# Performance work log

Measured on AMD Instinct MI355X. Metric: run time of the kernel, lower is better.

The kernel has to match this reference:

```python
import jax, jax.numpy as jnp
import numpy as np

N, D_IN, D_OUT = 8192, 768, 64

def setup_inputs() -> dict:
    key = jax.random.key(0)
    k1, k2, k3, k4 = jax.random.split(key, 4)
    x = jax.random.normal(k1, (N, D_IN), dtype=jnp.float32)
    # nn.Linear weight is [d_out, d_in]; we store transposed [d_in, d_out] for x @ W
    s = 1.0 / np.sqrt(D_IN)
    Wk = jax.random.normal(k2, (D_IN, D_OUT), dtype=jnp.float32) * s
    Wq = jax.random.normal(k3, (D_IN, D_OUT), dtype=jnp.float32) * s
    Wv = jax.random.normal(k4, (D_IN, D_OUT), dtype=jnp.float32) * s
    return {"x": x, "Wk": Wk, "Wq": Wq, "Wv": Wv}

def reference(x, Wk, Wq, Wv):
    inv_sqrt_dk = 1.0 / np.sqrt(D_OUT)
    # Faithful to source: k_w output used as the left matrix, q_w output as right
    wq = x @ Wk            # [N, d_out]  (source: weighted_q = k_w(x))
    wk = x @ Wq            # [N, d_out]  (source: weighted_k = q_w(x))
    scores = wq @ wk.T     # [N, N]
    attn = jax.nn.softmax(scores * inv_sqrt_dk, axis=-1)
    wv = x @ Wv            # [N, d_out]
    return attn @ wv       # [N, d_out]
```

## Files before the change

kernel.cpp:

```cpp
#include <hip/hip_runtime.h>
#include <hip/hip_bf16.h>

#define NTOK 8192
#define DIN  768

typedef float  f32x4  __attribute__((ext_vector_type(4)));
typedef float  f32x16 __attribute__((ext_vector_type(16)));
typedef short  bf16x8 __attribute__((ext_vector_type(8)));

static __device__ __forceinline__ unsigned short f2bf(float f) {
  unsigned int u = __float_as_uint(f);
  u += 0x7FFFu + ((u >> 16) & 1u);
  return (unsigned short)(u >> 16);
}
static __device__ __forceinline__ unsigned cvt_pk(float lo, float hi) {
  unsigned r;
  asm("v_cvt_pk_bf16_f32 %0, %1, %2" : "=v"(r) : "v"(lo), "v"(hi));
  return r;
}
static __device__ __forceinline__ void pswap(unsigned &x, unsigned &y) {
  auto r = __builtin_amdgcn_permlane32_swap(x, y, false, false);
  x = r[0]; y = r[1];
}

union U4 { unsigned u[4]; bf16x8 v; uint4 q; };

__global__ __launch_bounds__(256) void prep_wf(
    const float* __restrict__ Wk, const float* __restrict__ Wq,
    const float* __restrict__ Wv, unsigned short* __restrict__ Wf) {
  int tid  = blockIdx.x * 256 + threadIdx.x;
  int lane = tid & 63;
  int chunk = tid >> 6;
  int g = chunk / 24, kt = chunk - g * 24;
  int col = (g & 3) * 16 + (lane & 15);
  int k0  = kt * 32 + ((lane >> 4) & 3) * 8;
  int ws  = g >> 2;
  const float* W = (ws == 0) ? Wk : (ws == 1) ? Wq : Wv;
  U4 o;
#pragma unroll
  for (int jj = 0; jj < 4; ++jj)
    o.u[jj] = cvt_pk(W[(k0 + 2 * jj) * 64 + col], W[(k0 + 2 * jj + 1) * 64 + col]);
  *(uint4*)(Wf + (size_t)tid * 8) = o.q;
}

__global__ __launch_bounds__(384) void proj_qkv(
    const float* __restrict__ x, const unsigned short* __restrict__ Wf,
    unsigned short* __restrict__ Qb, unsigned short* __restrict__ Kf,
    unsigned short* __restrict__ Vf) {
  __shared__ uint4 xl4[16 * 96];
  int tid = threadIdx.x;
  int rowBase = blockIdx.x * 16;

#pragma unroll
  for (int s = 0; s < 4; ++s) {
    int idx = s * 384 + tid;
    int row = idx / 96, b = idx - row * 96;
    const float4* xp = (const float4*)(x + (size_t)(rowBase + row) * DIN + b * 8);
    float4 v0 = xp[0], v1 = xp[1];
    U4 o;
    o.u[0] = cvt_pk(v0.x, v0.y); o.u[1] = cvt_pk(v0.z, v0.w);
    o.u[2] = cvt_pk(v1.x, v1.y); o.u[3] = cvt_pk(v1.z, v1.w);
    xl4[row * 96 + (b ^ (row & 7))] = o.q;
  }
  __syncthreads();

  int wv = tid >> 6, lane = tid & 63;
  int r = lane & 15, hi = lane >> 4;
  int g0 = wv * 2;

  f32x4 acc[2];
  acc[0] = (f32x4){0.f, 0.f, 0.f, 0.f};
  acc[1] = (f32x4){0.f, 0.f, 0.f, 0.f};

  const bf16x8* xfr = (const bf16x8*)xl4;
#pragma unroll 4
  for (int kt = 0; kt < 24; ++kt) {
    bf16x8 af = xfr[r * 96 + ((kt * 4 + hi) ^ (r & 7))];
#pragma unroll
    for (int c = 0; c < 2; ++c) {
      bf16x8 wf = *(const bf16x8*)(Wf + ((size_t)((g0 + c) * 24 + kt) * 64 + lane) * 8);
      acc[c] = __builtin_amdgcn_mfma_f32_16x16x32_bf16(af, wf, acc[c], 0, 0, 0);
    }
  }

#pragma unroll
  for (int c = 0; c < 2; ++c) {
    int g  = g0 + c;
    int W  = g >> 2;
    int cc = (g & 3) * 16 + r;
    if (W == 0) {
#pragma unroll
      for (int i = 0; i < 4; ++i)
        Qb[(rowBase + hi * 4 + i) * 64 + cc] = f2bf(acc[c][i] * 0.125f);
    } else if (W == 1) {
      int cbit = cc >> 4, hb = (cc >> 3) & 1, j = cc & 7;
#pragma unroll
      for (int i = 0; i < 4; ++i) {
        int grow = rowBase + hi * 4 + i;
        Kf[(((size_t)(grow >> 5) * 4 + cbit) * 64 + (grow & 31) + 32 * hb) * 8 + j] =
            f2bf(acc[c][i]);
      }
    } else {
      int grow0 = rowBase + hi * 4;
      int T  = grow0 >> 5, ks = (grow0 >> 4) & 1;
      int dh = cc >> 5;
      int hb = (hi >> 1) & 1, j0 = (hi & 1) * 4;
      size_t addr = (((size_t)T * 4 + dh * 2 + ks) * 64 + (cc & 31) + 32 * hb) * 8 + j0;
      uint2 pk = {cvt_pk(acc[c][0], acc[c][1]), cvt_pk(acc[c][2], acc[c][3])};
      *(uint2*)(Vf + addr) = pk;
    }
  }
}

__global__ __launch_bounds__(1024, 4) void attn_kernel(
    const unsigned short* __restrict__ Qb, const unsigned short* __restrict__ Kf,
    const unsigned short* __restrict__ Vf, float* __restrict__ out) {
  __shared__ __align__(16) float Opart[16][32][64];
  __shared__ float Lden[16][2][32];

  int wv   = threadIdx.x >> 6;
  int lane = threadIdx.x & 63;
  int l31 = lane & 31, hi = lane >> 5;
  int q0 = blockIdx.x * 32;

  bf16x8 qf[4];
#pragma unroll
  for (int c = 0; c < 4; ++c)
    qf[c] = *(const bf16x8*)(Qb + (size_t)(q0 + l31) * 64 + c * 16 + hi * 8);

  f32x16 acc0, acc1;
#pragma unroll
  for (int i = 0; i < 16; ++i) { acc0[i] = 0.f; acc1[i] = 0.f; }
  float rsum = 0.f;

  const unsigned short* kf_l = Kf + (size_t)lane * 8;
  const unsigned short* vf_l = Vf + (size_t)lane * 8;

#pragma unroll 2
  for (int t = 0; t < 16; ++t) {
    int T = wv * 16 + t;
    const unsigned short* kc = kf_l + (size_t)T * 2048;
    bf16x8 kf0 = *(const bf16x8*)(kc);
    bf16x8 kf1 = *(const bf16x8*)(kc + 512);
    bf16x8 kf2 = *(const bf16x8*)(kc + 1024);
    bf16x8 kf3 = *(const bf16x8*)(kc + 1536);
    const unsigned short* vc = vf_l + (size_t)T * 2048;
    bf16x8 vf00 = *(const bf16x8*)(vc);
    bf16x8 vf01 = *(const bf16x8*)(vc + 512);
    bf16x8 vf10 = *(const bf16x8*)(vc + 1024);
    bf16x8 vf11 = *(const bf16x8*)(vc + 1536);

    f32x16 s;
#pragma unroll
    for (int i = 0; i < 16; ++i) s[i] = 0.f;
    s = __builtin_amdgcn_mfma_f32_32x32x16_bf16(kf0, qf[0], s, 0, 0, 0);
    s = __builtin_amdgcn_mfma_f32_32x32x16_bf16(kf1, qf[1], s, 0, 0, 0);
    s = __builtin_amdgcn_mfma_f32_32x32x16_bf16(kf2, qf[2], s, 0, 0, 0);
    s = __builtin_amdgcn_mfma_f32_32x32x16_bf16(kf3, qf[3], s, 0, 0, 0);

    float p[16];
#pragma unroll
    for (int i = 0; i < 16; ++i) {
      p[i] = __expf(s[i] - 12.0f);
      rsum += p[i];
    }

    unsigned a0 = cvt_pk(p[0], p[1]),   b0 = cvt_pk(p[4], p[5]);
    pswap(a0, b0);
    unsigned c0 = cvt_pk(p[2], p[3]),   d0 = cvt_pk(p[6], p[7]);
    pswap(c0, d0);
    unsigned a1 = cvt_pk(p[8], p[9]),   b1 = cvt_pk(p[12], p[13]);
    pswap(a1, b1);
    unsigned c1 = cvt_pk(p[10], p[11]), d1 = cvt_pk(p[14], p[15]);
    pswap(c1, d1);
    U4 pa0, pa1;
    pa0.u[0] = a0; pa0.u[1] = c0; pa0.u[2] = b0; pa0.u[3] = d0;
    pa1.u[0] = a1; pa1.u[1] = c1; pa1.u[2] = b1; pa1.u[3] = d1;

    acc0 = __builtin_amdgcn_mfma_f32_32x32x16_bf16(pa0.v, vf00, acc0, 0, 0, 0);
    acc1 = __builtin_amdgcn_mfma_f32_32x32x16_bf16(pa0.v, vf10, acc1, 0, 0, 0);
    acc0 = __builtin_amdgcn_mfma_f32_32x32x16_bf16(pa1.v, vf01, acc0, 0, 0, 0);
    acc1 = __builtin_amdgcn_mfma_f32_32x32x16_bf16(pa1.v, vf11, acc1, 0, 0, 0);
  }

#pragma unroll
  for (int rg = 0; rg < 16; ++rg) {
    int qr = (rg & 3) + 8 * (rg >> 2) + 4 * hi;
    Opart[wv][qr][l31]      = acc0[rg];
    Opart[wv][qr][32 + l31] = acc1[rg];
  }
  Lden[wv][hi][l31] = rsum;
  __syncthreads();

  int t  = threadIdx.x;
  int q  = t >> 5;
  int c2 = (t & 31) * 2;
  float den = 0.f;
#pragma unroll
  for (int w = 0; w < 16; ++w) den += Lden[w][0][q] + Lden[w][1][q];
  float nx = 0.f, ny = 0.f;
#pragma unroll
  for (int w = 0; w < 16; ++w) {
    float2 o = *(const float2*)&Opart[w][q][c2];
    nx += o.x; ny += o.y;
  }
  float inv = 1.f / den;
  float2 res = {nx * inv, ny * inv};
  *(float2*)(out + (size_t)(q0 + q) * 64 + c2) = res;
}

extern "C" void kernel_launch(void* const* d_in, const int* in_sizes, int n_in,
                              void* d_out, int out_size, void* d_ws, size_t ws_size,
                              hipStream_t stream) {
  const float* x  = (const float*)d_in[0];
  const float* Wk = (const float*)d_in[1];
  const float* Wq = (const float*)d_in[2];
  const float* Wv = (const float*)d_in[3];

  unsigned short* Qb = (unsigned short*)d_ws;
  unsigned short* Kf = Qb + (size_t)NTOK * 64;
  unsigned short* Vf = Kf + (size_t)NTOK * 64;
  unsigned short* Wf = Vf + (size_t)NTOK * 64;

  prep_wf<<<72, 256, 0, stream>>>(Wk, Wq, Wv, Wf);
  proj_qkv<<<NTOK / 16, 384, 0, stream>>>(x, Wf, Qb, Kf, Vf);
  attn_kernel<<<NTOK / 32, 1024, 0, stream>>>(Qb, Kf, Vf, (float*)d_out);
}
```

Measured before the change: 108.2 us.

## Restructure attention into split-K blocks sharing LDS-staged K/V with a separate reduction

The attention kernel changes from one block per 32 queries, where each wave streamed its own K/V slice from global memory, to blocks of 128 queries by 2048 keys. Each block stages shared K/V tiles in double-buffered LDS so four query sub-tiles reuse them. Partial numerators and denominators go to workspace and a new reduce_out kernel combines the four key splits. The projection kernel also moves to 768 threads with one output group per wave. This cuts repeated global K/V traffic, but adds per-iteration barriers, extra partial-sum global writes and reads, and one more launch.

Result: slower. 113.1 us (+4.5%).

```diff
diff --git a/kernel.cpp b/kernel.cpp
--- a/kernel.cpp
+++ b/kernel.cpp
@@ -43,7 +43,7 @@
   *(uint4*)(Wf + (size_t)tid * 8) = o.q;
 }
 
-__global__ __launch_bounds__(384) void proj_qkv(
+__global__ __launch_bounds__(768) void proj_qkv(
     const float* __restrict__ x, const unsigned short* __restrict__ Wf,
     unsigned short* __restrict__ Qb, unsigned short* __restrict__ Kf,
     unsigned short* __restrict__ Vf) {
@@ -52,8 +52,8 @@
   int rowBase = blockIdx.x * 16;
 
 #pragma unroll
-  for (int s = 0; s < 4; ++s) {
-    int idx = s * 384 + tid;
+  for (int s = 0; s < 2; ++s) {
+    int idx = s * 768 + tid;
     int row = idx / 96, b = idx - row * 96;
     const float4* xp = (const float4*)(x + (size_t)(rowBase + row) * DIN + b * 8);
     float4 v0 = xp[0], v1 = xp[1];
@@ -66,89 +66,106 @@
 
   int wv = tid >> 6, lane = tid & 63;
   int r = lane & 15, hi = lane >> 4;
-  int g0 = wv * 2;
-
-  f32x4 acc[2];
-  acc[0] = (f32x4){0.f, 0.f, 0.f, 0.f};
-  acc[1] = (f32x4){0.f, 0.f, 0.f, 0.f};
-
+
+  f32x4 acc = (f32x4){0.f, 0.f, 0.f, 0.f};
   const bf16x8* xfr = (const bf16x8*)xl4;
 #pragma unroll 4
   for (int kt = 0; kt < 24; ++kt) {
     bf16x8 af = xfr[r * 96 + ((kt * 4 + hi) ^ (r & 7))];
-#pragma unroll
-    for (int c = 0; c < 2; ++c) {
-      bf16x8 wf = *(const bf16x8*)(Wf + ((size_t)((g0 + c) * 24 + kt) * 64 + lane) * 8);
-      acc[c] = __builtin_amdgcn_mfma_f32_16x16x32_bf16(af, wf, acc[c], 0, 0, 0);
-    }
-  }
-
-#pragma unroll
-  for (int c = 0; c < 2; ++c) {
-    int g  = g0 + c;
-    int W  = g >> 2;
-    int cc = (g & 3) * 16 + r;
-    if (W == 0) {
-#pragma unroll
-      for (int i = 0; i < 4; ++i)
-        Qb[(rowBase + hi * 4 + i) * 64 + cc] = f2bf(acc[c][i] * 0.125f);
-    } else if (W == 1) {
-      int cbit = cc >> 4, hb = (cc >> 3) & 1, j = cc & 7;
-#pragma unroll
-      for (int i = 0; i < 4; ++i) {
-        int grow = rowBase + hi * 4 + i;
-        Kf[(((size_t)(grow >> 5) * 4 + cbit) * 64 + (grow & 31) + 32 * hb) * 8 + j] =
-            f2bf(acc[c][i]);
-      }
-    } else {
-      int grow0 = rowBase + hi * 4;
-      int T  = grow0 >> 5, ks = (grow0 >> 4) & 1;
-      int dh = cc >> 5;
-      int hb = (hi >> 1) & 1, j0 = (hi & 1) * 4;
-      size_t addr = (((size_t)T * 4 + dh * 2 + ks) * 64 + (cc & 31) + 32 * hb) * 8 + j0;
-      uint2 pk = {cvt_pk(acc[c][0], acc[c][1]), cvt_pk(acc[c][2], acc[c][3])};
-      *(uint2*)(Vf + addr) = pk;
-    }
+    bf16x8 wf = *(const bf16x8*)(Wf + ((size_t)(wv * 24 + kt) * 64 + lane) * 8);
+    acc = __builtin_amdgcn_mfma_f32_16x16x32_bf16(af, wf, acc, 0, 0, 0);
+  }
+
+  int g  = wv;
+  int W  = g >> 2;
+  int cc = (g & 3) * 16 + r;
+  if (W == 0) {
+#pragma unroll
+    for (int i = 0; i < 4; ++i)
+      Qb[(rowBase + hi * 4 + i) * 64 + cc] = f2bf(acc[i] * 0.125f);
+  } else if (W == 1) {
+    int cbit = cc >> 4, hb = (cc >> 3) & 1, j = cc & 7;
+#pragma unroll
+    for (int i = 0; i < 4; ++i) {
+      int grow = rowBase + hi * 4 + i;
+      Kf[(((size_t)(grow >> 5) * 4 + cbit) * 64 + (grow & 31) + 32 * hb) * 8 + j] =
+          f2bf(acc[i]);
+    }
+  } else {
+    int grow0 = rowBase + hi * 4;
+    int T  = grow0 >> 5, ks = (grow0 >> 4) & 1;
+    int dh = cc >> 5;
+    int hb = (hi >> 1) & 1, j0 = (hi & 1) * 4;
+    size_t addr = (((size_t)T * 4 + dh * 2 + ks) * 64 + (cc & 31) + 32 * hb) * 8 + j0;
+    uint2 pk = {cvt_pk(acc[0], acc[1]), cvt_pk(acc[2], acc[3])};
+    *(uint2*)(Vf + addr) = pk;
   }
 }
 
 __global__ __launch_bounds__(1024, 4) void attn_kernel(
     const unsigned short* __restrict__ Qb, const unsigned short* __restrict__ Kf,
-    const unsigned short* __restrict__ Vf, float* __restrict__ out) {
-  __shared__ __align__(16) float Opart[16][32][64];
-  __shared__ float Lden[16][2][32];
+    const unsigned short* __restrict__ Vf, float* __restrict__ Pnum,
+    float* __restrict__ Pden) {
+  __shared__ unsigned short kvbuf[2][32][512];
+
+  int bid  = blockIdx.x;
+  int orig = (bid & 7) * 32 + (bid >> 3);
+  int kb   = orig >> 6;
+  int qt   = orig & 63;
 
   int wv   = threadIdx.x >> 6;
+  int qs   = wv >> 2;
+  int ks   = wv & 3;
   int lane = threadIdx.x & 63;
   int l31 = lane & 31, hi = lane >> 5;
-  int q0 = blockIdx.x * 32;
+  int q0g  = qt * 128 + qs * 32;
 
   bf16x8 qf[4];
 #pragma unroll
   for (int c = 0; c < 4; ++c)
-    qf[c] = *(const bf16x8*)(Qb + (size_t)(q0 + l31) * 64 + c * 16 + hi * 8);
+    qf[c] = *(const bf16x8*)(Qb + (size_t)(q0g + l31) * 64 + c * 16 + hi * 8);
 
   f32x16 acc0, acc1;
 #pragma unroll
   for (int i = 0; i < 16; ++i) { acc0[i] = 0.f; acc1[i] = 0.f; }
   float rsum = 0.f;
 
-  const unsigned short* kf_l = Kf + (size_t)lane * 8;
-  const unsigned short* vf_l = Vf + (size_t)lane * 8;
+  int cc0 = wv * 2, cc1 = cc0 + 1;
+  int ksc0 = cc0 >> 3, kv0 = (cc0 >> 2) & 1, sl0 = cc0 & 3;
+  int ksc1 = cc1 >> 3, kv1 = (cc1 >> 2) & 1, sl1 = cc1 & 3;
+  const unsigned short* s0 =
+      (kv0 ? Vf : Kf) + ((size_t)(kb * 64 + ksc0 * 16) * 2048) + sl0 * 512 + (size_t)lane * 8;
+  const unsigned short* s1 =
+      (kv1 ? Vf : Kf) + ((size_t)(kb * 64 + ksc1 * 16) * 2048) + sl1 * 512 + (size_t)lane * 8;
+
+  {
+    uint4 a = *(const uint4*)s0;
+    uint4 b = *(const uint4*)s1;
+    *(uint4*)(&kvbuf[0][cc0][0] + lane * 8) = a;
+    *(uint4*)(&kvbuf[0][cc1][0] + lane * 8) = b;
+  }
+  __syncthreads();
+
+  const unsigned short* rb0 = &kvbuf[0][ks * 8][0] + (size_t)lane * 8;
 
 #pragma unroll 2
   for (int t = 0; t < 16; ++t) {
-    int T = wv * 16 + t;
-    const unsigned short* kc = kf_l + (size_t)T * 2048;
-    bf16x8 kf0 = *(const bf16x8*)(kc);
-    bf16x8 kf1 = *(const bf16x8*)(kc + 512);
-    bf16x8 kf2 = *(const bf16x8*)(kc + 1024);
-    bf16x8 kf3 = *(const bf16x8*)(kc + 1536);
-    const unsigned short* vc = vf_l + (size_t)T * 2048;
-    bf16x8 vf00 = *(const bf16x8*)(vc);
-    bf16x8 vf01 = *(const bf16x8*)(vc + 512);
-    bf16x8 vf10 = *(const bf16x8*)(vc + 1024);
-    bf16x8 vf11 = *(const bf16x8*)(vc + 1536);
+    int cur = t & 1;
+    uint4 ga, gb;
+    if (t < 15) {
+      ga = *(const uint4*)(s0 + (size_t)(t + 1) * 2048);
+      gb = *(const uint4*)(s1 + (size_t)(t + 1) * 2048);
+    }
+
+    const unsigned short* kbse = rb0 + (size_t)cur * 16384;
+    bf16x8 kf0 = *(const bf16x8*)(kbse);
+    bf16x8 kf1 = *(const bf16x8*)(kbse + 512);
+    bf16x8 kf2 = *(const bf16x8*)(kbse + 1024);
+    bf16x8 kf3 = *(const bf16x8*)(kbse + 1536);
+    bf16x8 vf00 = *(const bf16x8*)(kbse + 2048);
+    bf16x8 vf01 = *(const bf16x8*)(kbse + 2560);
+    bf16x8 vf10 = *(const bf16x8*)(kbse + 3072);
+    bf16x8 vf11 = *(const bf16x8*)(kbse + 3584);
 
     f32x16 s;
 #pragma unroll
@@ -181,32 +198,43 @@
     acc1 = __builtin_amdgcn_mfma_f32_32x32x16_bf16(pa0.v, vf10, acc1, 0, 0, 0);
     acc0 = __builtin_amdgcn_mfma_f32_32x32x16_bf16(pa1.v, vf01, acc0, 0, 0, 0);
     acc1 = __builtin_amdgcn_mfma_f32_32x32x16_bf16(pa1.v, vf11, acc1, 0, 0, 0);
-  }
-
+
+    if (t < 15) {
+      *(uint4*)(&kvbuf[cur ^ 1][cc0][0] + lane * 8) = ga;
+      *(uint4*)(&kvbuf[cur ^ 1][cc1][0] + lane * 8) = gb;
+    }
+    __syncthreads();
+  }
+
+  int pidx = kb * 4 + ks;
 #pragma unroll
   for (int rg = 0; rg < 16; ++rg) {
     int qr = (rg & 3) + 8 * (rg >> 2) + 4 * hi;
-    Opart[wv][qr][l31]      = acc0[rg];
-    Opart[wv][qr][32 + l31] = acc1[rg];
-  }
-  Lden[wv][hi][l31] = rsum;
-  __syncthreads();
-
-  int t  = threadIdx.x;
-  int q  = t >> 5;
-  int c2 = (t & 31) * 2;
+    size_t base = ((size_t)pidx * NTOK + q0g + qr) * 64;
+    Pnum[base + l31]      = acc0[rg];
+    Pnum[base + 32 + l31] = acc1[rg];
+  }
+  float rtot = rsum + __shfl_xor(rsum, 32);
+  if (hi == 0) Pden[(size_t)pidx * NTOK + q0g + l31] = rtot;
+}
+
+__global__ __launch_bounds__(256) void reduce_out(
+    const float* __restrict__ Pnum, const float* __restrict__ Pden,
+    float* __restrict__ out) {
+  int gid = blockIdx.x * 256 + threadIdx.x;
+  int q  = gid >> 4;
+  int c4 = (gid & 15) * 4;
+  float4 n = {0.f, 0.f, 0.f, 0.f};
   float den = 0.f;
 #pragma unroll
-  for (int w = 0; w < 16; ++w) den += Lden[w][0][q] + Lden[w][1][q];
-  float nx = 0.f, ny = 0.f;
-#pragma unroll
-  for (int w = 0; w < 16; ++w) {
-    float2 o = *(const float2*)&Opart[w][q][c2];
-    nx += o.x; ny += o.y;
+  for (int p = 0; p < 16; ++p) {
+    float4 o = *(const float4*)(Pnum + ((size_t)p * NTOK + q) * 64 + c4);
+    n.x += o.x; n.y += o.y; n.z += o.z; n.w += o.w;
+    den += Pden[(size_t)p * NTOK + q];
   }
   float inv = 1.f / den;
-  float2 res = {nx * inv, ny * inv};
-  *(float2*)(out + (size_t)(q0 + q) * 64 + c2) = res;
+  float4 res = {n.x * inv, n.y * inv, n.z * inv, n.w * inv};
+  *(float4*)(out + (size_t)q * 64 + c4) = res;
 }
 
 extern "C" void kernel_launch(void* const* d_in, const int* in_sizes, int n_in,
@@ -221,8 +249,11 @@
   unsigned short* Kf = Qb + (size_t)NTOK * 64;
   unsigned short* Vf = Kf + (size_t)NTOK * 64;
   unsigned short* Wf = Vf + (size_t)NTOK * 64;
+  float* Pnum = (float*)((char*)d_ws + (8u << 20));
+  float* Pden = (float*)((char*)d_ws + (40u << 20));
 
   prep_wf<<<72, 256, 0, stream>>>(Wk, Wq, Wv, Wf);
-  proj_qkv<<<NTOK / 16, 384, 0, stream>>>(x, Wf, Qb, Kf, Vf);
-  attn_kernel<<<NTOK / 32, 1024, 0, stream>>>(Qb, Kf, Vf, (float*)d_out);
-}
+  proj_qkv<<<NTOK / 16, 768, 0, stream>>>(x, Wf, Qb, Kf, Vf);
+  attn_kernel<<<256, 1024, 0, stream>>>(Qb, Kf, Vf, Pnum, Pden);
+  reduce_out<<<512, 256, 0, stream>>>(Pnum, Pden, (float*)d_out);
+}
```
